# Kernel tuning notes

Hardware: AMD Instinct MI355X
Metric: run time of the kernel (lower is better)

## Reference

```python
import jax, jax.numpy as jnp
import numpy as np

D_MODEL = 1024
N_HEAD = 16
N_KV_HEAD = 4
HEAD_DIM = D_MODEL // N_HEAD  # 64
N_GROUP = N_HEAD // N_KV_HEAD  # 4
ROPE_BASE = 10000.0
ROPE_DIM = HEAD_DIM  # rope_percentage = 1.0


def _rope_tables(seq_len, dtype):
    half = ROPE_DIM // 2
    inv_freq = 1.0 / (ROPE_BASE ** (jnp.arange(0, half, dtype=jnp.float32) * 2.0 / ROPE_DIM))
    pos = jnp.arange(seq_len, dtype=jnp.float32)
    freqs = pos[:, None] * inv_freq[None, :]  # [S, half]
    return jnp.cos(freqs).astype(dtype), jnp.sin(freqs).astype(dtype)


def _apply_rope(t):
    # t: [B, H, S, D]; rotate first ROPE_DIM dims (split-half convention)
    S = t.shape[2]
    cos, sin = _rope_tables(S, t.dtype)  # [S, half]
    half = ROPE_DIM // 2
    t1 = t[..., :half]
    t2 = t[..., half:ROPE_DIM]
    rot = jnp.concatenate([t1 * cos - t2 * sin, t1 * sin + t2 * cos], axis=-1)
    if ROPE_DIM < t.shape[-1]:
        rot = jnp.concatenate([rot, t[..., ROPE_DIM:]], axis=-1)
    return rot


def setup_inputs() -> dict:
    key = jax.random.key(0)
    ks = jax.random.split(key, 5)
    B, S = 1, 4096
    sd = 1.0 / np.sqrt(D_MODEL)
    x = jax.random.normal(ks[0], (B, S, D_MODEL), dtype=jnp.float32)
    w_q = jax.random.normal(ks[1], (D_MODEL, N_HEAD * HEAD_DIM), dtype=jnp.float32) * sd
    w_k = jax.random.normal(ks[2], (D_MODEL, N_KV_HEAD * HEAD_DIM), dtype=jnp.float32) * sd
    w_v = jax.random.normal(ks[3], (D_MODEL, N_KV_HEAD * HEAD_DIM), dtype=jnp.float32) * sd
    w_o = jax.random.normal(ks[4], (D_MODEL, D_MODEL), dtype=jnp.float32) * sd
    return {"x": x, "w_q": w_q, "w_k": w_k, "w_v": w_v, "w_o": w_o}


def reference(x, w_q, w_k, w_v, w_o):
    B, S, _ = x.shape
    q = (x @ w_q).reshape(B, S, N_HEAD, HEAD_DIM).transpose(0, 2, 1, 3)     # [B,H,S,D]
    k = (x @ w_k).reshape(B, S, N_KV_HEAD, HEAD_DIM).transpose(0, 2, 1, 3)  # [B,Hk,S,D]
    v = (x @ w_v).reshape(B, S, N_KV_HEAD, HEAD_DIM).transpose(0, 2, 1, 3)
    q = _apply_rope(q)
    k = _apply_rope(k)
    # repeat KV heads to match query heads (ops.repeat along head axis)
    k = jnp.repeat(k, N_GROUP, axis=1)  # [B,H,S,D]
    v = jnp.repeat(v, N_GROUP, axis=1)
    scale = 1.0 / jnp.sqrt(jnp.asarray(HEAD_DIM, dtype=x.dtype))
    scores = jnp.einsum("bhqd,bhkd->bhqk", q, k) * scale
    attn = jax.nn.softmax(scores, axis=-1)
    out = jnp.einsum("bhqk,bhkd->bhqd", attn, v)  # [B,H,S,D]
    out = out.transpose(0, 2, 1, 3).reshape(B, S, D_MODEL)
    return out @ w_o
```

## Files before the change

kernel.cpp:

```cpp
#include <hip/hip_runtime.h>
#include <hip/hip_bf16.h>
#include <math.h>

#define S_LEN 4096
#define DMODEL 1024
#define NHEAD 16
#define NKV 4
#define HDIM 64
#define QSCALE 0.18033688011112042f

typedef __attribute__((ext_vector_type(8))) short bf16x8;
typedef __attribute__((ext_vector_type(4))) float f32x4;

static __device__ __forceinline__ unsigned short f2bf(float f) {
  unsigned int u = __float_as_uint(f);
  u += 0x7fffu + ((u >> 16) & 1u);
  return (unsigned short)(u >> 16);
}

static __device__ __forceinline__ unsigned short f2bf_hw(float f) {
  union { __hip_bfloat16 h; unsigned short u; } cv;
  cv.h = __float2bfloat16(f);
  return cv.u;
}

static __device__ __forceinline__ float fexp2(float x) {
  return __builtin_amdgcn_exp2f(x);
}

static __device__ __forceinline__ void gload_lds16(const unsigned short* g, unsigned short* l) {
  __builtin_amdgcn_global_load_lds((const __attribute__((address_space(1))) void*)g,
                                   (__attribute__((address_space(3))) void*)l, 16, 0, 0);
}

__global__ void k_cast4(const float* __restrict__ in, unsigned short* __restrict__ out) {
  int i = blockIdx.x * blockDim.x + threadIdx.x;
  if (i >= S_LEN * DMODEL / 4) return;
  f32x4 v = *(const f32x4*)(in + (size_t)i * 4);
  union { unsigned short us[4]; uint2 d; } o;
#pragma unroll
  for (int j = 0; j < 4; ++j) o.us[j] = f2bf(v[j]);
  *(uint2*)(out + (size_t)i * 4) = o.d;
}

__global__ __launch_bounds__(256) void k_prepw(const float* __restrict__ wq, const float* __restrict__ wk,
                                               const float* __restrict__ wv, const float* __restrict__ wo,
                                               unsigned short* __restrict__ wqkvT, unsigned short* __restrict__ woT) {
  __shared__ float T[64][65];
  int b = blockIdx.x;
  const float* src;
  unsigned short* dst;
  int srcN, n0, k0, scol;
  if (b < 384) {
    int rt = b >> 4, kt = b & 15;
    n0 = rt * 64; k0 = kt * 64;
    if (n0 < 1024) { src = wq; srcN = 1024; scol = n0; }
    else if (n0 < 1280) { src = wk; srcN = 256; scol = n0 - 1024; }
    else { src = wv; srcN = 256; scol = n0 - 1280; }
    dst = wqkvT;
  } else {
    int bb = b - 384;
    int rt = bb >> 4, kt = bb & 15;
    n0 = rt * 64; k0 = kt * 64;
    src = wo; srcN = 1024; scol = n0; dst = woT;
  }
  int tr = threadIdx.x >> 6, tc = threadIdx.x & 63;
#pragma unroll
  for (int i = 0; i < 16; ++i) {
    int kk = i * 4 + tr;
    T[kk][tc] = src[(size_t)(k0 + kk) * srcN + scol + tc];
  }
  __syncthreads();
#pragma unroll
  for (int i = 0; i < 16; ++i) {
    int nn = i * 4 + tr;
    dst[(size_t)(n0 + nn) * 1024 + k0 + tc] = f2bf(T[tc][nn]);
  }
}

__global__ void k_rope_tables(float* __restrict__ ct, float* __restrict__ st) {
  int i = blockIdx.x * blockDim.x + threadIdx.x;
  if (i >= S_LEN * 32) return;
  int s = i >> 5, d = i & 31;
  float inv = expf(-(float)d * (1.0f / 32.0f) * logf(10000.0f));
  float f = (float)s * inv;
  ct[i] = cosf(f);
  st[i] = sinf(f);
}

__global__ __launch_bounds__(256) void k_gemmQKV(const unsigned short* __restrict__ A,
                                                 const unsigned short* __restrict__ BT,
                                                 const float* __restrict__ ct, const float* __restrict__ st,
                                                 unsigned short* __restrict__ Qb, unsigned short* __restrict__ Kh,
                                                 unsigned short* __restrict__ VP) {
  __shared__ unsigned short As[128 * 64];
  __shared__ unsigned short Bs[128 * 64];
  const int tid = threadIdx.x;
  const int lane = tid & 63, wid = tid >> 6;
  const int r = lane & 15, g = lane >> 4;
  const int wm = wid >> 1, wn = wid & 1;
  const int bn0 = blockIdx.x << 7;
  const int bm0 = blockIdx.y << 7;

  f32x4 acc[4][4];
#pragma unroll
  for (int mt = 0; mt < 4; ++mt)
#pragma unroll
    for (int nt = 0; nt < 4; ++nt) acc[mt][nt] = 0.0f;

  for (int k0 = 0; k0 < 1024; k0 += 64) {
#pragma unroll
    for (int i = 0; i < 4; ++i) {
      int c = i * 256 + tid;
      int row = c >> 3, slot = c & 7;
      int ss = slot ^ (row & 7);
      int lbase = (i * 256 + (tid & ~63)) * 8;
      gload_lds16(A + (size_t)(bm0 + row) * 1024 + k0 + ss * 8, &As[lbase]);
      gload_lds16(BT + (size_t)(bn0 + row) * 1024 + k0 + ss * 8, &Bs[lbase]);
    }
    __syncthreads();
#pragma unroll
    for (int h = 0; h < 2; ++h) {
      bf16x8 am[4], bn[4];
#pragma unroll
      for (int mt = 0; mt < 4; ++mt) {
        int row = wm * 64 + mt * 16 + r;
        int slot = (g + 4 * h) ^ (row & 7);
        am[mt] = *(const bf16x8*)&As[row * 64 + slot * 8];
      }
#pragma unroll
      for (int nt = 0; nt < 4; ++nt) {
        int row = wn * 64 + nt * 16 + r;
        int slot = (g + 4 * h) ^ (row & 7);
        bn[nt] = *(const bf16x8*)&Bs[row * 64 + slot * 8];
      }
#pragma unroll
      for (int mt = 0; mt < 4; ++mt)
#pragma unroll
        for (int nt = 0; nt < 4; ++nt)
          acc[mt][nt] = __builtin_amdgcn_mfma_f32_16x16x32_bf16(am[mt], bn[nt], acc[mt][nt], 0, 0, 0);
    }
    __syncthreads();
  }

  const int colbase = bn0 + wn * 64;
  const int srow0 = bm0 + wm * 64;
  if (colbase < 1024) {
#pragma unroll
    for (int mt = 0; mt < 4; ++mt)
#pragma unroll
      for (int q = 0; q < 4; ++q) {
        int srow = srow0 + mt * 16 + g * 4 + q;
#pragma unroll
        for (int ntp = 0; ntp < 2; ++ntp) {
          int di = ntp * 16 + r;
          float t1 = acc[mt][ntp][q], t2 = acc[mt][ntp + 2][q];
          float c = ct[srow * 32 + di], s = st[srow * 32 + di];
          Qb[(size_t)srow * 1024 + colbase + di] = f2bf((t1 * c - t2 * s) * QSCALE);
          Qb[(size_t)srow * 1024 + colbase + di + 32] = f2bf((t1 * s + t2 * c) * QSCALE);
        }
      }
  } else if (colbase < 1280) {
    const int kvh = (colbase - 1024) >> 6;
#pragma unroll
    for (int mt = 0; mt < 4; ++mt)
#pragma unroll
      for (int q = 0; q < 4; ++q) {
        int srow = srow0 + mt * 16 + g * 4 + q;
#pragma unroll
        for (int ntp = 0; ntp < 2; ++ntp) {
          int di = ntp * 16 + r;
          float t1 = acc[mt][ntp][q], t2 = acc[mt][ntp + 2][q];
          float c = ct[srow * 32 + di], s = st[srow * 32 + di];
          Kh[((size_t)kvh * S_LEN + srow) * 64 + di] = f2bf(t1 * c - t2 * s);
          Kh[((size_t)kvh * S_LEN + srow) * 64 + di + 32] = f2bf(t1 * s + t2 * c);
        }
      }
  } else {
    const int vcol = colbase - 1280;
    const int kvh = vcol >> 6;
    unsigned short* vdst = VP + (size_t)kvh * HDIM * S_LEN;
#pragma unroll
    for (int mt = 0; mt < 4; ++mt)
#pragma unroll
      for (int q = 0; q < 4; ++q) {
        int srow = srow0 + mt * 16 + g * 4 + q;
        int k = srow & 63;
        int sperm = (srow & ~63) + 32 * (k >> 5) + 8 * ((k >> 2) & 3) + 4 * ((k >> 4) & 1) + (k & 3);
#pragma unroll
        for (int nt = 0; nt < 4; ++nt)
          vdst[(size_t)(nt * 16 + r) * S_LEN + sperm] = f2bf(acc[mt][nt][q]);
      }
  }
}

__global__ __launch_bounds__(256) void k_gemm128(const unsigned short* __restrict__ A,
                                                 const unsigned short* __restrict__ BT,
                                                 float* __restrict__ C, int M, int N, int K) {
  __shared__ unsigned short As[128 * 64];
  __shared__ unsigned short Bs[128 * 64];
  const int tid = threadIdx.x;
  const int lane = tid & 63, wid = tid >> 6;
  const int r = lane & 15, g = lane >> 4;
  const int wm = wid >> 1, wn = wid & 1;
  const int bn0 = blockIdx.x << 7;
  const int bm0 = blockIdx.y << 7;

  f32x4 acc[4][4];
#pragma unroll
  for (int mt = 0; mt < 4; ++mt)
#pragma unroll
    for (int nt = 0; nt < 4; ++nt) acc[mt][nt] = 0.0f;

  for (int k0 = 0; k0 < K; k0 += 64) {
#pragma unroll
    for (int i = 0; i < 4; ++i) {
      int c = i * 256 + tid;
      int row = c >> 3, slot = c & 7;
      int ss = slot ^ (row & 7);
      int lbase = (i * 256 + (tid & ~63)) * 8;
      gload_lds16(A + (size_t)(bm0 + row) * K + k0 + ss * 8, &As[lbase]);
      gload_lds16(BT + (size_t)(bn0 + row) * K + k0 + ss * 8, &Bs[lbase]);
    }
    __syncthreads();
#pragma unroll
    for (int h = 0; h < 2; ++h) {
      bf16x8 am[4], bn[4];
#pragma unroll
      for (int mt = 0; mt < 4; ++mt) {
        int row = wm * 64 + mt * 16 + r;
        int slot = (g + 4 * h) ^ (row & 7);
        am[mt] = *(const bf16x8*)&As[row * 64 + slot * 8];
      }
#pragma unroll
      for (int nt = 0; nt < 4; ++nt) {
        int row = wn * 64 + nt * 16 + r;
        int slot = (g + 4 * h) ^ (row & 7);
        bn[nt] = *(const bf16x8*)&Bs[row * 64 + slot * 8];
      }
#pragma unroll
      for (int mt = 0; mt < 4; ++mt)
#pragma unroll
        for (int nt = 0; nt < 4; ++nt)
          acc[mt][nt] = __builtin_amdgcn_mfma_f32_16x16x32_bf16(am[mt], bn[nt], acc[mt][nt], 0, 0, 0);
    }
    __syncthreads();
  }
#pragma unroll
  for (int mt = 0; mt < 4; ++mt)
#pragma unroll
    for (int nt = 0; nt < 4; ++nt)
#pragma unroll
      for (int q = 0; q < 4; ++q)
        C[(size_t)(bm0 + wm * 64 + mt * 16 + g * 4 + q) * N + bn0 + wn * 64 + nt * 16 + r] = acc[mt][nt][q];
}

__global__ __launch_bounds__(256, 4) void k_attn(const unsigned short* __restrict__ Q,
                                                 const unsigned short* __restrict__ Kh,
                                                 const unsigned short* __restrict__ VP,
                                                 unsigned short* __restrict__ Ab) {
  __shared__ unsigned short sm[2][2][4096];
  const int tid = threadIdx.x;
  const int wave = tid >> 6, lane = tid & 63;
  const int r = lane & 15, g = lane >> 4;
  const int bid = blockIdx.x;
  const int kvh = bid & 3;
  const int qbase = (((bid >> 3) << 1) + ((bid >> 2) & 1)) * 16;
  const int head = kvh * 4 + wave;
  const int bidx = (lane & 48) >> 2;

  const unsigned short* khb = Kh + (size_t)kvh * S_LEN * 64;
  const unsigned short* vpb = VP + (size_t)kvh * S_LEN * 64;

  bf16x8 qf[2];
#pragma unroll
  for (int h0 = 0; h0 < 2; ++h0)
    qf[h0] = *(const bf16x8*)(Q + (size_t)(qbase + r) * DMODEL + head * HDIM + 32 * h0 + 8 * g);

  f32x4 Oa[4];
#pragma unroll
  for (int dt = 0; dt < 4; ++dt) Oa[dt] = 0.0f;
  float l_ = 0.0f;

  auto stage = [&](int b, int kv0) {
#pragma unroll
    for (int i = 0; i < 2; ++i) {
      int row = i * 32 + (tid >> 3), slot = tid & 7;
      int cs = slot ^ (row & 7);
      int lbase = (i * 256 + (tid & ~63)) * 8;
      gload_lds16(khb + (size_t)(kv0 + row) * 64 + cs * 8, &sm[b][0][lbase]);
      gload_lds16(vpb + (size_t)row * S_LEN + kv0 + cs * 8, &sm[b][1][lbase]);
    }
  };

  stage(0, 0);
  asm volatile("s_waitcnt vmcnt(0)" ::: "memory");
  __syncthreads();

  for (int t = 0; t < 64; ++t) {
    const int buf = t & 1;
    if (t < 63) stage(buf ^ 1, (t + 1) * 64);

    bf16x8 kf[4][2], vf[4][2];
#pragma unroll
    for (int tt = 0; tt < 4; ++tt) {
      int row = 16 * tt + r;
#pragma unroll
      for (int h = 0; h < 2; ++h) {
        int slot = (g + 4 * h) ^ (r & 7);
        kf[tt][h] = *(const bf16x8*)&sm[buf][0][row * 64 + slot * 8];
        vf[tt][h] = *(const bf16x8*)&sm[buf][1][row * 64 + slot * 8];
      }
    }
    f32x4 sc[4];
#pragma unroll
    for (int tt = 0; tt < 4; ++tt) {
      f32x4 a = 0.0f;
      a = __builtin_amdgcn_mfma_f32_16x16x32_bf16(kf[tt][0], qf[0], a, 0, 0, 0);
      a = __builtin_amdgcn_mfma_f32_16x16x32_bf16(kf[tt][1], qf[1], a, 0, 0, 0);
      sc[tt] = a;
    }
    float s0 = 0.f, s1 = 0.f, s2 = 0.f, s3 = 0.f;
#pragma unroll
    for (int p = 0; p < 4; ++p) {
      sc[0][p] = fexp2(sc[0][p]); s0 += sc[0][p];
      sc[1][p] = fexp2(sc[1][p]); s1 += sc[1][p];
      sc[2][p] = fexp2(sc[2][p]); s2 += sc[2][p];
      sc[3][p] = fexp2(sc[3][p]); s3 += sc[3][p];
    }
    l_ += (s0 + s1) + (s2 + s3);
    bf16x8 pa[2];
#pragma unroll
    for (int u = 0; u < 2; ++u) {
      union { bf16x8 v; unsigned short us[8]; } pk;
#pragma unroll
      for (int j = 0; j < 4; ++j) {
        pk.us[j] = f2bf_hw(sc[2 * u][j]);
        pk.us[4 + j] = f2bf_hw(sc[2 * u + 1][j]);
      }
      pa[u] = pk.v;
    }
#pragma unroll
    for (int dt = 0; dt < 4; ++dt) {
      Oa[dt] = __builtin_amdgcn_mfma_f32_16x16x32_bf16(pa[0], vf[dt][0], Oa[dt], 0, 0, 0);
      Oa[dt] = __builtin_amdgcn_mfma_f32_16x16x32_bf16(pa[1], vf[dt][1], Oa[dt], 0, 0, 0);
    }
    asm volatile("s_waitcnt vmcnt(0)" ::: "memory");
    __syncthreads();
  }
  float lt = l_;
  lt += __shfl_xor(lt, 16, 64);
  lt += __shfl_xor(lt, 32, 64);
  float li = 1.0f / lt;
  float bl[4];
#pragma unroll
  for (int p = 0; p < 4; ++p) bl[p] = __shfl(li, bidx + p, 64);
#pragma unroll
  for (int dt = 0; dt < 4; ++dt)
#pragma unroll
    for (int p = 0; p < 4; ++p)
      Ab[(size_t)(qbase + 4 * g + p) * DMODEL + head * HDIM + 16 * dt + r] =
          f2bf(Oa[dt][p] * bl[p]);
}

extern "C" void kernel_launch(void* const* d_in, const int* in_sizes, int n_in,
                              void* d_out, int out_size, void* d_ws, size_t ws_size,
                              hipStream_t stream) {
  const float* x   = (const float*)d_in[0];
  const float* w_q = (const float*)d_in[1];
  const float* w_k = (const float*)d_in[2];
  const float* w_v = (const float*)d_in[3];
  const float* w_o = (const float*)d_in[4];
  float* out = (float*)d_out;

  char* ws = (char*)d_ws;
  size_t off = 0;
  auto alloc = [&](size_t bytes) -> void* {
    void* p = ws + off;
    off = (off + bytes + 255) & ~(size_t)255;
    return p;
  };
  unsigned short* xb    = (unsigned short*)alloc((size_t)S_LEN * DMODEL * 2);
  unsigned short* wqkvT = (unsigned short*)alloc((size_t)1536 * DMODEL * 2);
  unsigned short* woT   = (unsigned short*)alloc((size_t)DMODEL * DMODEL * 2);
  float* ct = (float*)alloc((size_t)S_LEN * 32 * 4);
  float* st = (float*)alloc((size_t)S_LEN * 32 * 4);
  unsigned short* Qb = (unsigned short*)alloc((size_t)S_LEN * DMODEL * 2);
  unsigned short* Kh = (unsigned short*)alloc((size_t)NKV * S_LEN * HDIM * 2);
  unsigned short* VP = (unsigned short*)alloc((size_t)NKV * HDIM * S_LEN * 2);
  unsigned short* Ab = (unsigned short*)alloc((size_t)S_LEN * DMODEL * 2);

  k_cast4<<<(S_LEN * DMODEL / 4 + 255) / 256, 256, 0, stream>>>(x, xb);
  k_prepw<<<640, 256, 0, stream>>>(w_q, w_k, w_v, w_o, wqkvT, woT);
  k_rope_tables<<<(S_LEN * 32 + 255) / 256, 256, 0, stream>>>(ct, st);

  k_gemmQKV<<<dim3(1536 / 128, S_LEN / 128), 256, 0, stream>>>(xb, wqkvT, ct, st, Qb, Kh, VP);

  k_attn<<<1024, 256, 0, stream>>>(Qb, Kh, VP, Ab);

  k_gemm128<<<dim3(DMODEL / 128, S_LEN / 128), 256, 0, stream>>>(Ab, woT, out, S_LEN, DMODEL, DMODEL);
}
```

Before: 213.9 us.

## Double-buffer GEMM LDS tiles and merge prep kernels into one launch

Both bf16 GEMM kernels now use two LDS buffers, so the global-to-LDS load of the next K tile is issued before the MFMA work on the current tile, hiding load latency behind compute. This doubles LDS use per block to 64KB, which can lower occupancy. The three prep kernels (x cast, weight transpose/cast, rope tables) are merged into one launch split by block index, removing two kernel launches.

```diff
diff --git a/kernel.cpp b/kernel.cpp
--- a/kernel.cpp
+++ b/kernel.cpp
@@ -33,59 +33,62 @@
                                    (__attribute__((address_space(3))) void*)l, 16, 0, 0);
 }
 
-__global__ void k_cast4(const float* __restrict__ in, unsigned short* __restrict__ out) {
-  int i = blockIdx.x * blockDim.x + threadIdx.x;
-  if (i >= S_LEN * DMODEL / 4) return;
-  f32x4 v = *(const f32x4*)(in + (size_t)i * 4);
-  union { unsigned short us[4]; uint2 d; } o;
-#pragma unroll
-  for (int j = 0; j < 4; ++j) o.us[j] = f2bf(v[j]);
-  *(uint2*)(out + (size_t)i * 4) = o.d;
-}
-
-__global__ __launch_bounds__(256) void k_prepw(const float* __restrict__ wq, const float* __restrict__ wk,
-                                               const float* __restrict__ wv, const float* __restrict__ wo,
-                                               unsigned short* __restrict__ wqkvT, unsigned short* __restrict__ woT) {
+__global__ __launch_bounds__(256) void k_prep(const float* __restrict__ x,
+                                              const float* __restrict__ wq, const float* __restrict__ wk,
+                                              const float* __restrict__ wv, const float* __restrict__ wo,
+                                              unsigned short* __restrict__ xb,
+                                              unsigned short* __restrict__ wqkvT, unsigned short* __restrict__ woT,
+                                              float* __restrict__ ct, float* __restrict__ st) {
   __shared__ float T[64][65];
-  int b = blockIdx.x;
-  const float* src;
-  unsigned short* dst;
-  int srcN, n0, k0, scol;
-  if (b < 384) {
-    int rt = b >> 4, kt = b & 15;
-    n0 = rt * 64; k0 = kt * 64;
-    if (n0 < 1024) { src = wq; srcN = 1024; scol = n0; }
-    else if (n0 < 1280) { src = wk; srcN = 256; scol = n0 - 1024; }
-    else { src = wv; srcN = 256; scol = n0 - 1280; }
-    dst = wqkvT;
+  const int b = blockIdx.x;
+  if (b < 640) {
+    const float* src;
+    unsigned short* dst;
+    int srcN, n0, k0, scol;
+    if (b < 384) {
+      int rt = b >> 4, kt = b & 15;
+      n0 = rt * 64; k0 = kt * 64;
+      if (n0 < 1024) { src = wq; srcN = 1024; scol = n0; }
+      else if (n0 < 1280) { src = wk; srcN = 256; scol = n0 - 1024; }
+      else { src = wv; srcN = 256; scol = n0 - 1280; }
+      dst = wqkvT;
+    } else {
+      int bb = b - 384;
+      int rt = bb >> 4, kt = bb & 15;
+      n0 = rt * 64; k0 = kt * 64;
+      src = wo; srcN = 1024; scol = n0; dst = woT;
+    }
+    int tr = threadIdx.x >> 6, tc = threadIdx.x & 63;
+#pragma unroll
+    for (int i = 0; i < 16; ++i) {
+      int kk = i * 4 + tr;
+      T[kk][tc] = src[(size_t)(k0 + kk) * srcN + scol + tc];
+    }
+    __syncthreads();
+#pragma unroll
+    for (int i = 0; i < 16; ++i) {
+      int nn = i * 4 + tr;
+      dst[(size_t)(n0 + nn) * 1024 + k0 + tc] = f2bf(T[tc][nn]);
+    }
+  } else if (b < 1152) {
+    int i = (b - 640) * 256 + threadIdx.x;
+    if (i < S_LEN * 32) {
+      int s = i >> 5, d = i & 31;
+      float inv = expf(-(float)d * (1.0f / 32.0f) * logf(10000.0f));
+      float f = (float)s * inv;
+      ct[i] = cosf(f);
+      st[i] = sinf(f);
+    }
   } else {
-    int bb = b - 384;
-    int rt = bb >> 4, kt = bb & 15;
-    n0 = rt * 64; k0 = kt * 64;
-    src = wo; srcN = 1024; scol = n0; dst = woT;
+    int i = (b - 1152) * 256 + threadIdx.x;
+    if (i < S_LEN * DMODEL / 4) {
+      f32x4 v = *(const f32x4*)(x + (size_t)i * 4);
+      union { unsigned short us[4]; uint2 d; } o;
+#pragma unroll
+      for (int j = 0; j < 4; ++j) o.us[j] = f2bf(v[j]);
+      *(uint2*)(xb + (size_t)i * 4) = o.d;
+    }
   }
-  int tr = threadIdx.x >> 6, tc = threadIdx.x & 63;
-#pragma unroll
-  for (int i = 0; i < 16; ++i) {
-    int kk = i * 4 + tr;
-    T[kk][tc] = src[(size_t)(k0 + kk) * srcN + scol + tc];
-  }
-  __syncthreads();
-#pragma unroll
-  for (int i = 0; i < 16; ++i) {
-    int nn = i * 4 + tr;
-    dst[(size_t)(n0 + nn) * 1024 + k0 + tc] = f2bf(T[tc][nn]);
-  }
-}
-
-__global__ void k_rope_tables(float* __restrict__ ct, float* __restrict__ st) {
-  int i = blockIdx.x * blockDim.x + threadIdx.x;
-  if (i >= S_LEN * 32) return;
-  int s = i >> 5, d = i & 31;
-  float inv = expf(-(float)d * (1.0f / 32.0f) * logf(10000.0f));
-  float f = (float)s * inv;
-  ct[i] = cosf(f);
-  st[i] = sinf(f);
 }
 
 __global__ __launch_bounds__(256) void k_gemmQKV(const unsigned short* __restrict__ A,
@@ -93,8 +96,8 @@
                                                  const float* __restrict__ ct, const float* __restrict__ st,
                                                  unsigned short* __restrict__ Qb, unsigned short* __restrict__ Kh,
                                                  unsigned short* __restrict__ VP) {
-  __shared__ unsigned short As[128 * 64];
-  __shared__ unsigned short Bs[128 * 64];
+  __shared__ unsigned short As[2][128 * 64];
+  __shared__ unsigned short Bs[2][128 * 64];
   const int tid = threadIdx.x;
   const int lane = tid & 63, wid = tid >> 6;
   const int r = lane & 15, g = lane >> 4;
@@ -108,17 +111,25 @@
 #pragma unroll
     for (int nt = 0; nt < 4; ++nt) acc[mt][nt] = 0.0f;
 
-  for (int k0 = 0; k0 < 1024; k0 += 64) {
+  auto stage = [&](int bsel, int k0) {
 #pragma unroll
     for (int i = 0; i < 4; ++i) {
       int c = i * 256 + tid;
       int row = c >> 3, slot = c & 7;
       int ss = slot ^ (row & 7);
       int lbase = (i * 256 + (tid & ~63)) * 8;
-      gload_lds16(A + (size_t)(bm0 + row) * 1024 + k0 + ss * 8, &As[lbase]);
-      gload_lds16(BT + (size_t)(bn0 + row) * 1024 + k0 + ss * 8, &Bs[lbase]);
-    }
-    __syncthreads();
+      gload_lds16(A + (size_t)(bm0 + row) * 1024 + k0 + ss * 8, &As[bsel][lbase]);
+      gload_lds16(BT + (size_t)(bn0 + row) * 1024 + k0 + ss * 8, &Bs[bsel][lbase]);
+    }
+  };
+
+  stage(0, 0);
+  asm volatile("s_waitcnt vmcnt(0)" ::: "memory");
+  __syncthreads();
+
+  for (int t = 0; t < 16; ++t) {
+    const int buf = t & 1;
+    if (t < 15) stage(buf ^ 1, (t + 1) * 64);
 #pragma unroll
     for (int h = 0; h < 2; ++h) {
       bf16x8 am[4], bn[4];
@@ -126,13 +137,13 @@
       for (int mt = 0; mt < 4; ++mt) {
         int row = wm * 64 + mt * 16 + r;
         int slot = (g + 4 * h) ^ (row & 7);
-        am[mt] = *(const bf16x8*)&As[row * 64 + slot * 8];
+        am[mt] = *(const bf16x8*)&As[buf][row * 64 + slot * 8];
       }
 #pragma unroll
       for (int nt = 0; nt < 4; ++nt) {
         int row = wn * 64 + nt * 16 + r;
         int slot = (g + 4 * h) ^ (row & 7);
-        bn[nt] = *(const bf16x8*)&Bs[row * 64 + slot * 8];
+        bn[nt] = *(const bf16x8*)&Bs[buf][row * 64 + slot * 8];
       }
 #pragma unroll
       for (int mt = 0; mt < 4; ++mt)
@@ -140,6 +151,7 @@
         for (int nt = 0; nt < 4; ++nt)
           acc[mt][nt] = __builtin_amdgcn_mfma_f32_16x16x32_bf16(am[mt], bn[nt], acc[mt][nt], 0, 0, 0);
     }
+    asm volatile("s_waitcnt vmcnt(0)" ::: "memory");
     __syncthreads();
   }
 
@@ -197,8 +209,8 @@
 __global__ __launch_bounds__(256) void k_gemm128(const unsigned short* __restrict__ A,
                                                  const unsigned short* __restrict__ BT,
                                                  float* __restrict__ C, int M, int N, int K) {
-  __shared__ unsigned short As[128 * 64];
-  __shared__ unsigned short Bs[128 * 64];
+  __shared__ unsigned short As[2][128 * 64];
+  __shared__ unsigned short Bs[2][128 * 64];
   const int tid = threadIdx.x;
   const int lane = tid & 63, wid = tid >> 6;
   const int r = lane & 15, g = lane >> 4;
@@ -212,17 +224,26 @@
 #pragma unroll
     for (int nt = 0; nt < 4; ++nt) acc[mt][nt] = 0.0f;
 
-  for (int k0 = 0; k0 < K; k0 += 64) {
+  auto stage = [&](int bsel, int k0) {
 #pragma unroll
     for (int i = 0; i < 4; ++i) {
       int c = i * 256 + tid;
       int row = c >> 3, slot = c & 7;
       int ss = slot ^ (row & 7);
       int lbase = (i * 256 + (tid & ~63)) * 8;
-      gload_lds16(A + (size_t)(bm0 + row) * K + k0 + ss * 8, &As[lbase]);
-      gload_lds16(BT + (size_t)(bn0 + row) * K + k0 + ss * 8, &Bs[lbase]);
-    }
-    __syncthreads();
+      gload_lds16(A + (size_t)(bm0 + row) * K + k0 + ss * 8, &As[bsel][lbase]);
+      gload_lds16(BT + (size_t)(bn0 + row) * K + k0 + ss * 8, &Bs[bsel][lbase]);
+    }
+  };
+
+  stage(0, 0);
+  asm volatile("s_waitcnt vmcnt(0)" ::: "memory");
+  __syncthreads();
+
+  const int nk = K >> 6;
+  for (int t = 0; t < nk; ++t) {
+    const int buf = t & 1;
+    if (t < nk - 1) stage(buf ^ 1, (t + 1) * 64);
 #pragma unroll
     for (int h = 0; h < 2; ++h) {
       bf16x8 am[4], bn[4];
@@ -230,13 +251,13 @@
       for (int mt = 0; mt < 4; ++mt) {
         int row = wm * 64 + mt * 16 + r;
         int slot = (g + 4 * h) ^ (row & 7);
-        am[mt] = *(const bf16x8*)&As[row * 64 + slot * 8];
+        am[mt] = *(const bf16x8*)&As[buf][row * 64 + slot * 8];
       }
 #pragma unroll
       for (int nt = 0; nt < 4; ++nt) {
         int row = wn * 64 + nt * 16 + r;
         int slot = (g + 4 * h) ^ (row & 7);
-        bn[nt] = *(const bf16x8*)&Bs[row * 64 + slot * 8];
+        bn[nt] = *(const bf16x8*)&Bs[buf][row * 64 + slot * 8];
       }
 #pragma unroll
       for (int mt = 0; mt < 4; ++mt)
@@ -244,6 +265,7 @@
         for (int nt = 0; nt < 4; ++nt)
           acc[mt][nt] = __builtin_amdgcn_mfma_f32_16x16x32_bf16(am[mt], bn[nt], acc[mt][nt], 0, 0, 0);
     }
+    asm volatile("s_waitcnt vmcnt(0)" ::: "memory");
     __syncthreads();
   }
 #pragma unroll
@@ -390,9 +412,7 @@
   unsigned short* VP = (unsigned short*)alloc((size_t)NKV * HDIM * S_LEN * 2);
   unsigned short* Ab = (unsigned short*)alloc((size_t)S_LEN * DMODEL * 2);
 
-  k_cast4<<<(S_LEN * DMODEL / 4 + 255) / 256, 256, 0, stream>>>(x, xb);
-  k_prepw<<<640, 256, 0, stream>>>(w_q, w_k, w_v, w_o, wqkvT, woT);
-  k_rope_tables<<<(S_LEN * 32 + 255) / 256, 256, 0, stream>>>(ct, st);
+  k_prep<<<5248, 256, 0, stream>>>(x, w_q, w_k, w_v, w_o, xb, wqkvT, woT, ct, st);
 
   k_gemmQKV<<<dim3(1536 / 128, S_LEN / 128), 256, 0, stream>>>(xb, wqkvT, ct, st, Qb, Kh, VP);
 
```

Result: faster. 207.5 us (-3.0%).
